# Kernel tuning notes

Hardware: AMD Instinct MI355X
Metric: run time of the kernel (lower is better)

The kernel has to match this reference:

```python
import jax, jax.numpy as jnp
import numpy as np

# ---- fixed problem dims (match init_kwargs) ----
B = 256            # graph pairs
NQ, NC = 96, 120   # nodes per query / corpus graph
EQ, EC = 192, 240  # edges per query / corpus graph
M = 256            # max_edge_set_size (pad target)
RAW = 32           # raw node/edge feature dim
H = 64             # node_state_dim
MSG = 128          # message_dim == encoded edge dim
SDIM = 64          # sinkhorn_feature_dim
PROP_STEPS = 3
TIME_STEPS = 2
SINK_ITERS = 10
TEMP = 0.1
N_NODES = B * (NQ + NC)
N_EDGES = B * (EQ + EC)


def _mlp2(x, W1, b1, W2, b2):
    return jax.nn.relu(x @ W1 + b1) @ W2 + b2


def _split_and_stack(ef):
    # edges laid out [q0, c0, q1, c1, ...]; pad each graph's edges to M
    D = ef.shape[-1]
    ef = ef.reshape(B, EQ + EC, D)
    q = jnp.pad(ef[:, :EQ], ((0, 0), (0, M - EQ), (0, 0)))
    c = jnp.pad(ef[:, EQ:], ((0, 0), (0, M - EC), (0, 0)))
    return q, c


def _sinkhorn(log_alpha):
    la = log_alpha / TEMP
    for _ in range(SINK_ITERS):
        la = la - jax.nn.logsumexp(la, axis=2, keepdims=True)
        la = la - jax.nn.logsumexp(la, axis=1, keepdims=True)
    return jnp.exp(la)


def setup_inputs() -> dict:
    key = jax.random.key(0)
    ks = jax.random.split(key, 16)
    rng = np.random.default_rng(0)
    nodes_per_graph = np.tile(np.array([NQ, NC]), B)            # [2B]
    node_offsets = np.concatenate([[0], np.cumsum(nodes_per_graph)[:-1]])
    edges_per_graph = np.tile(np.array([EQ, EC]), B)
    eg = np.repeat(np.arange(2 * B), edges_per_graph)           # graph id per edge
    from_idx = node_offsets[eg] + rng.integers(0, nodes_per_graph[eg])
    to_idx = node_offsets[eg] + rng.integers(0, nodes_per_graph[eg])

    def lin(k, i, o):
        return (jax.random.normal(k, (i, o), jnp.float32) / np.sqrt(i)).astype(jnp.float32)

    return {
        "node_features": jax.random.normal(ks[0], (N_NODES, RAW), jnp.float32),
        "edge_features": jax.random.normal(ks[1], (N_EDGES, RAW), jnp.float32),
        "from_idx": jnp.asarray(from_idx, jnp.int32),
        "to_idx": jnp.asarray(to_idx, jnp.int32),
        "enc_node_W": lin(ks[2], RAW, H), "enc_node_b": jnp.zeros((H,), jnp.float32),
        "enc_edge_W": lin(ks[3], RAW, MSG), "enc_edge_b": jnp.zeros((MSG,), jnp.float32),
        "msg_W1": lin(ks[4], 2 * H + MSG, 2 * MSG), "msg_b1": jnp.zeros((2 * MSG,), jnp.float32),
        "msg_W2": lin(ks[5], 2 * MSG, MSG), "msg_b2": jnp.zeros((MSG,), jnp.float32),
        "upd_W1": lin(ks[6], H + 2 * MSG, 2 * H), "upd_b1": jnp.zeros((2 * H,), jnp.float32),
        "upd_W2": lin(ks[7], 2 * H, H), "upd_b2": jnp.zeros((H,), jnp.float32),
        "int_W1": lin(ks[8], 2 * MSG, 2 * MSG), "int_b1": jnp.zeros((2 * MSG,), jnp.float32),
        "int_W2": lin(ks[9], 2 * MSG, MSG), "int_b2": jnp.zeros((MSG,), jnp.float32),
        "sink_W1": lin(ks[10], MSG, SDIM), "sink_b1": jnp.zeros((SDIM,), jnp.float32),
        "sink_W2": lin(ks[11], SDIM, SDIM), "sink_b2": jnp.zeros((SDIM,), jnp.float32),
    }


def _forward(node_features, edge_features,
             enc_node_W, enc_node_b, enc_edge_W, enc_edge_b,
             msg_W1, msg_b1, msg_W2, msg_b2,
             upd_W1, upd_b1, upd_W2, upd_b2,
             int_W1, int_b1, int_W2, int_b2,
             sink_W1, sink_b1, sink_W2, sink_b2,
             from_idx, to_idx):
    h0 = node_features @ enc_node_W + enc_node_b      # GraphEncoder (nodes)
    e0 = edge_features @ enc_edge_W + enc_edge_b      # GraphEncoder (edges) -> MSG dim
    mask_q = (jnp.arange(M) < EQ).astype(h0.dtype)[None, :, None]
    mask_c = (jnp.arange(M) < EC).astype(h0.dtype)[None, :, None]

    def edge_msgs(h, comb):
        hf, ht = h[from_idx], h[to_idx]
        mf = _mlp2(jnp.concatenate([hf, ht, comb], -1), msg_W1, msg_b1, msg_W2, msg_b2)
        mb = _mlp2(jnp.concatenate([ht, hf, comb], -1), msg_W1, msg_b1, msg_W2, msg_b2)
        return mf, mb

    plan = None
    q_store = c_store = None
    for _ in range(TIME_STEPS):
        h, e = h0, e0
        inter = jnp.zeros((N_EDGES, MSG), e0.dtype)
        for _ in range(PROP_STEPS):
            # interaction encoder on [edge_features_enc, interaction_features]
            comb = _mlp2(jnp.concatenate([e, inter], -1), int_W1, int_b1, int_W2, int_b2)
            # prop_layer: bidirectional messages + aggregation + node update
            mf, mb = edge_msgs(h, comb)
            agg_f = jax.ops.segment_sum(mf, to_idx, num_segments=N_NODES)
            agg_b = jax.ops.segment_sum(mb, from_idx, num_segments=N_NODES)
            h = _mlp2(jnp.concatenate([h, agg_f, agg_b], -1), upd_W1, upd_b1, upd_W2, upd_b2)
            # propagation_messages: per-edge messages from updated node states
            mf2, mb2 = edge_msgs(h, comb)
            e = mf2 + mb2
            # interaction features via transport-plan gather (zeros on first time step)
            if plan is None:
                inter = jnp.zeros((N_EDGES, MSG), e.dtype)
            else:
                qs, cs = _split_and_stack(e)
                q_int = jnp.einsum('bqc,bcd->bqd', plan, cs)[:, :EQ]
                c_int = jnp.einsum('bqc,bqd->bcd', plan, qs)[:, :EC]
                inter = jnp.concatenate([q_int, c_int], 1).reshape(N_EDGES, MSG)
        q_store, c_store = _split_and_stack(e)
        fq = _mlp2(q_store, sink_W1, sink_b1, sink_W2, sink_b2) * mask_q
        fc = _mlp2(c_store, sink_W1, sink_b1, sink_W2, sink_b2) * mask_c
        plan = _sinkhorn(jnp.einsum('bqd,bcd->bqc', fq, fc))
    # feature_alignment_score: -||Q - P C||_1 per pair
    return -jnp.abs(q_store - jnp.einsum('bqc,bcd->bqd', plan, c_store)).sum((1, 2))


def reference(node_features, edge_features, from_idx, to_idx,
              enc_node_W, enc_node_b, enc_edge_W, enc_edge_b,
              msg_W1, msg_b1, msg_W2, msg_b2,
              upd_W1, upd_b1, upd_W2, upd_b2,
              int_W1, int_b1, int_W2, int_b2,
              sink_W1, sink_b1, sink_W2, sink_b2):
    return _forward(node_features, edge_features,
                    enc_node_W, enc_node_b, enc_edge_W, enc_edge_b,
                    msg_W1, msg_b1, msg_W2, msg_b2,
                    upd_W1, upd_b1, upd_W2, upd_b2,
                    int_W1, int_b1, int_W2, int_b2,
                    sink_W1, sink_b1, sink_W2, sink_b2,
                    from_idx, to_idx)
```

## Files before the change

### kernel.cpp

```cpp
#include <hip/hip_runtime.h>
#include <math.h>

constexpr int BATCH = 256;
constexpr int EQ_   = 192;
constexpr int EC_   = 240;
constexpr int EPG   = 432;
constexpr int NPG   = 216;
constexpr int NN    = BATCH * NPG;
constexpr int NE    = BATCH * EPG;

typedef __attribute__((ext_vector_type(8))) short short8;
typedef __attribute__((ext_vector_type(4))) float floatx4;
typedef unsigned short u16;

__device__ __forceinline__ u16 f2bf(float x) {
  union { float f; unsigned u; } c; c.f = x;
  const unsigned r = (c.u + 0x7FFFu + ((c.u >> 16) & 1u)) >> 16;
  return (u16)r;
}
__device__ __forceinline__ float bf2f(u16 x) {
  union { unsigned u; float f; } c; c.u = ((unsigned)x) << 16;
  return c.f;
}
__device__ __forceinline__ unsigned pack2(float a, float b) {
  return (unsigned)f2bf(a) | ((unsigned)f2bf(b) << 16);
}
__device__ __forceinline__ short8 cvt8(const float* __restrict__ p) {
  const float4 a = *(const float4*)p;
  const float4 b = *(const float4*)(p + 4);
  short8 o;
  o[0]=(short)f2bf(a.x); o[1]=(short)f2bf(a.y); o[2]=(short)f2bf(a.z); o[3]=(short)f2bf(a.w);
  o[4]=(short)f2bf(b.x); o[5]=(short)f2bf(b.y); o[6]=(short)f2bf(b.z); o[7]=(short)f2bf(b.w);
  return o;
}

__device__ __forceinline__ void lse_online(float& m, float& s, float tt) {
  if (tt > m) { s = s * __expf(m - tt) + 1.f; m = tt; }
  else        { s += __expf(tt - m); }
}

__global__ __launch_bounds__(256)
void wconv(const float* __restrict__ W, u16* __restrict__ out, int K, int N)
{
  const int i = blockIdx.x * 256 + threadIdx.x;
  if (i < K * N) {
    const int n = i / K, k = i - n * K;
    out[i] = f2bf(W[(size_t)k * N + n]);
  }
}

template<int K1, int HID, int NOUT, int IN_MODE, int DUAL, int OUT_MODE, int WAVES>
__global__ __launch_bounds__(WAVES * 64, 4)
void mlp_mfma(const void* __restrict__ X, const void* __restrict__ P2,
              const void* __restrict__ P3, const u16* __restrict__ CB,
              const int* __restrict__ IA, const int* __restrict__ IB,
              const u16* __restrict__ W1t, const float* __restrict__ B1,
              const u16* __restrict__ W2t, const float* __restrict__ B2,
              float* __restrict__ Yf, u16* __restrict__ Yb0, u16* __restrict__ Yb1)
{
  constexpr int RT  = 32;
  constexpr int THREADS = WAVES * 64;
  constexpr int KCH = K1 / 8;
  constexpr int NT1 = HID / (WAVES * 16);
  constexpr int NT2 = (NOUT / (WAVES * 16) > 0) ? NOUT / (WAVES * 16) : 1;
  constexpr int SAB = RT * K1 * 2;
  constexpr int SHB = RT * (HID + 8) * 2;
  __shared__ __align__(16) char smem[(SAB > SHB ? SAB : SHB)];
  u16* sA = (u16*)smem;
  u16* sH = (u16*)smem;

  const int tid = threadIdx.x;
  const int rowBase = blockIdx.x * RT;

  for (int ch = tid; ch < RT * KCH; ch += THREADS) {
    const int r = ch / KCH, kc = ch - r * KCH;
    const int gr = rowBase + r, k0 = kc * 8;
    short8 pk;
    if constexpr (IN_MODE == 4) {
      const float* Xf  = (const float*)X;
      const float* P2f = (const float*)P2;
      if (k0 < 128)      pk = cvt8(&Xf[(size_t)gr * 128 + k0]);
      else if (P2f)      pk = cvt8(&P2f[(size_t)gr * 128 + (k0 - 128)]);
      else { pk = short8{0,0,0,0,0,0,0,0}; }
    } else if constexpr (IN_MODE == 1) {
      const u16* Hb = (const u16*)X;
      if (k0 < 64)       pk = *(const short8*)&Hb[(size_t)IA[gr] * 64 + k0];
      else if (k0 < 128) pk = *(const short8*)&Hb[(size_t)IB[gr] * 64 + (k0 - 64)];
      else               pk = *(const short8*)&CB[(size_t)gr * 128 + (k0 - 128)];
    } else {
      const u16* Hb = (const u16*)X;
      const u16* A0 = (const u16*)P2;
      const u16* A1 = (const u16*)P3;
      if (k0 < 64)       pk = *(const short8*)&Hb[(size_t)gr * 64 + k0];
      else if (k0 < 192) pk = *(const short8*)&A0[(size_t)gr * 128 + (k0 - 64)];
      else               pk = *(const short8*)&A1[(size_t)gr * 128 + (k0 - 192)];
    }
    const int byte = ((r * K1 + k0) * 2) ^ ((r & 7) << 4);
    *(short8*)((char*)sA + byte) = pk;
  }
  __syncthreads();

  const int wid = tid >> 6, lane = tid & 63;
  const int l15 = lane & 15, lg = lane >> 4;

  floatx4 acc1[1 + DUAL][2][NT1];
  #pragma unroll
  for (int d = 0; d <= DUAL; ++d)
    #pragma unroll
    for (int m = 0; m < 2; ++m)
      #pragma unroll
      for (int n = 0; n < NT1; ++n) acc1[d][m][n] = floatx4{0.f,0.f,0.f,0.f};

  #pragma unroll 2
  for (int kk = 0; kk < K1 / 32; ++kk) {
    short8 bw[NT1];
    #pragma unroll
    for (int n = 0; n < NT1; ++n) {
      const int col = wid * (HID / WAVES) + n * 16 + l15;
      bw[n] = *(const short8*)&W1t[(size_t)col * K1 + kk * 32 + lg * 8];
    }
    #pragma unroll
    for (int d = 0; d <= DUAL; ++d) {
      int k0 = kk * 32 + lg * 8;
      if (DUAL && d && k0 < 128) k0 ^= 64;
      #pragma unroll
      for (int m = 0; m < 2; ++m) {
        const int r = m * 16 + l15;
        const int byte = ((r * K1 + k0) * 2) ^ ((r & 7) << 4);
        const short8 af = *(const short8*)((char*)sA + byte);
        #pragma unroll
        for (int n = 0; n < NT1; ++n)
          acc1[d][m][n] = __builtin_amdgcn_mfma_f32_16x16x32_bf16(af, bw[n], acc1[d][m][n], 0, 0, 0);
      }
    }
  }
  __syncthreads();

  floatx4 accO[2][NT2];
  #pragma unroll
  for (int m = 0; m < 2; ++m)
    #pragma unroll
    for (int n = 0; n < NT2; ++n) accO[m][n] = floatx4{0.f,0.f,0.f,0.f};

  #pragma unroll
  for (int d = 0; d <= DUAL; ++d) {
    #pragma unroll
    for (int n = 0; n < NT1; ++n) {
      const int col = wid * (HID / WAVES) + n * 16 + l15;
      const float b1 = B1[col];
      #pragma unroll
      for (int m = 0; m < 2; ++m)
        #pragma unroll
        for (int r = 0; r < 4; ++r) {
          const int row = m * 16 + lg * 4 + r;
          const float y = acc1[d][m][n][r] + b1;
          sH[row * (HID + 8) + col] = f2bf(y > 0.f ? y : 0.f);
        }
    }
    __syncthreads();
    if (OUT_MODE == 2 && d == 1) {
      #pragma unroll
      for (int m = 0; m < 2; ++m)
        #pragma unroll
        for (int n = 0; n < NT2; ++n) accO[m][n] = floatx4{0.f,0.f,0.f,0.f};
    }
    #pragma unroll 2
    for (int kk = 0; kk < HID / 32; ++kk) {
      short8 bw2[NT2];
      #pragma unroll
      for (int n = 0; n < NT2; ++n) {
        const int col = wid * (NOUT / WAVES) + n * 16 + l15;
        bw2[n] = *(const short8*)&W2t[(size_t)col * HID + kk * 32 + lg * 8];
      }
      #pragma unroll
      for (int m = 0; m < 2; ++m) {
        const short8 af = *(const short8*)&sH[(m * 16 + l15) * (HID + 8) + kk * 32 + lg * 8];
        #pragma unroll
        for (int n = 0; n < NT2; ++n)
          accO[m][n] = __builtin_amdgcn_mfma_f32_16x16x32_bf16(af, bw2[n], accO[m][n], 0, 0, 0);
      }
    }
    if constexpr (OUT_MODE == 2) {
      u16* Y = d ? Yb1 : Yb0;
      #pragma unroll
      for (int n = 0; n < NT2; ++n) {
        const int col = wid * (NOUT / WAVES) + n * 16 + l15;
        const float b2 = B2[col];
        #pragma unroll
        for (int m = 0; m < 2; ++m)
          #pragma unroll
          for (int r = 0; r < 4; ++r) {
            const int gr = rowBase + m * 16 + lg * 4 + r;
            Y[(size_t)gr * NOUT + col] = f2bf(accO[m][n][r] + b2);
          }
      }
    }
    if (DUAL && d == 0) __syncthreads();
  }

  if constexpr (OUT_MODE != 2) {
    #pragma unroll
    for (int n = 0; n < NT2; ++n) {
      const int col = wid * (NOUT / WAVES) + n * 16 + l15;
      const float b2 = B2[col] * (float)(1 + DUAL);
      #pragma unroll
      for (int m = 0; m < 2; ++m)
        #pragma unroll
        for (int r = 0; r < 4; ++r) {
          const int gr = rowBase + m * 16 + lg * 4 + r;
          const float y = accO[m][n][r] + b2;
          if constexpr (OUT_MODE == 1) Yb0[(size_t)gr * NOUT + col] = f2bf(y);
          else                         Yf[(size_t)gr * NOUT + col] = y;
        }
    }
  }
}

__global__ __launch_bounds__(512, 4)
void comb_msg_fused(const float* __restrict__ E, const float* __restrict__ INTER,
                    const u16* __restrict__ Hb,
                    const int* __restrict__ IA, const int* __restrict__ IB,
                    const u16* __restrict__ Wi1, const float* __restrict__ Bi1,
                    const u16* __restrict__ Wi2, const float* __restrict__ Bi2,
                    const u16* __restrict__ Wm1, const float* __restrict__ Bm1,
                    const u16* __restrict__ Wm2, const float* __restrict__ Bm2,
                    u16* __restrict__ COMB, u16* __restrict__ MI )
{
  constexpr int RT = 32;
  __shared__ __align__(16) char smem[RT * (256 + 8) * 2];
  u16* sA = (u16*)smem;
  u16* sH = (u16*)smem;

  const int tid = threadIdx.x;
  const int rowBase = blockIdx.x * RT;
  const int wid = tid >> 6, lane = tid & 63;
  const int l15 = lane & 15, lg = lane >> 4;

  for (int ch = tid; ch < RT * 32; ch += 512) {
    const int r = ch >> 5, kc = ch & 31;
    const int gr = rowBase + r, k0 = kc * 8;
    short8 pk;
    if (k0 < 128)   pk = cvt8(&E[(size_t)gr * 128 + k0]);
    else if (INTER) pk = cvt8(&INTER[(size_t)gr * 128 + (k0 - 128)]);
    else            pk = short8{0,0,0,0,0,0,0,0};
    const int byte = ((r * 256 + k0) * 2) ^ ((r & 7) << 4);
    *(short8*)((char*)sA + byte) = pk;
  }
  __syncthreads();

  floatx4 c1[2][2];
  #pragma unroll
  for (int m = 0; m < 2; ++m) { c1[m][0] = floatx4{0,0,0,0}; c1[m][1] = floatx4{0,0,0,0}; }
  #pragma unroll 2
  for (int kk = 0; kk < 8; ++kk) {
    short8 bw[2];
    #pragma unroll
    for (int n = 0; n < 2; ++n) {
      const int col = wid * 32 + n * 16 + l15;
      bw[n] = *(const short8*)&Wi1[(size_t)col * 256 + kk * 32 + lg * 8];
    }
    #pragma unroll
    for (int m = 0; m < 2; ++m) {
      const int r = m * 16 + l15;
      const int byte = ((r * 256 + kk * 32 + lg * 8) * 2) ^ ((r & 7) << 4);
      const short8 af = *(const short8*)((char*)sA + byte);
      c1[m][0] = __builtin_amdgcn_mfma_f32_16x16x32_bf16(af, bw[0], c1[m][0], 0, 0, 0);
      c1[m][1] = __builtin_amdgcn_mfma_f32_16x16x32_bf16(af, bw[1], c1[m][1], 0, 0, 0);
    }
  }
  __syncthreads();
  #pragma unroll
  for (int n = 0; n < 2; ++n) {
    const int col = wid * 32 + n * 16 + l15;
    const float b1 = Bi1[col];
    #pragma unroll
    for (int m = 0; m < 2; ++m)
      #pragma unroll
      for (int r = 0; r < 4; ++r) {
        const int row = m * 16 + lg * 4 + r;
        const float y = c1[m][n][r] + b1;
        sH[row * 264 + col] = f2bf(y > 0.f ? y : 0.f);
      }
  }
  __syncthreads();
  floatx4 cO[2];
  cO[0] = floatx4{0,0,0,0}; cO[1] = floatx4{0,0,0,0};
  #pragma unroll 2
  for (int kk = 0; kk < 8; ++kk) {
    const int col = wid * 16 + l15;
    const short8 bw2 = *(const short8*)&Wi2[(size_t)col * 256 + kk * 32 + lg * 8];
    #pragma unroll
    for (int m = 0; m < 2; ++m) {
      const short8 af = *(const short8*)&sH[(m * 16 + l15) * 264 + kk * 32 + lg * 8];
      cO[m] = __builtin_amdgcn_mfma_f32_16x16x32_bf16(af, bw2, cO[m], 0, 0, 0);
    }
  }
  __syncthreads();

  {
    const int col = wid * 16 + l15;
    const float b2 = Bi2[col];
    #pragma unroll
    for (int m = 0; m < 2; ++m)
      #pragma unroll
      for (int r = 0; r < 4; ++r) {
        const int row = m * 16 + lg * 4 + r;
        const int gr = rowBase + row;
        const u16 v = f2bf(cO[m][r] + b2);
        COMB[(size_t)gr * 128 + col] = v;
        const int k0 = 128 + col;
        const int byte = ((row * 256 + k0) * 2) ^ ((row & 7) << 4);
        *(u16*)((char*)sA + byte) = v;
      }
  }
  for (int ch = tid; ch < RT * 16; ch += 512) {
    const int r = ch >> 4, kc = ch & 15;
    const int gr = rowBase + r, k0 = kc * 8;
    short8 pk;
    if (k0 < 64) pk = *(const short8*)&Hb[(size_t)IA[gr] * 64 + k0];
    else         pk = *(const short8*)&Hb[(size_t)IB[gr] * 64 + (k0 - 64)];
    const int byte = ((r * 256 + k0) * 2) ^ ((r & 7) << 4);
    *(short8*)((char*)sA + byte) = pk;
  }
  __syncthreads();

  floatx4 m1[2][2][2];
  #pragma unroll
  for (int d = 0; d < 2; ++d)
    #pragma unroll
    for (int m = 0; m < 2; ++m) { m1[d][m][0] = floatx4{0,0,0,0}; m1[d][m][1] = floatx4{0,0,0,0}; }
  #pragma unroll 2
  for (int kk = 0; kk < 8; ++kk) {
    short8 bw[2];
    #pragma unroll
    for (int n = 0; n < 2; ++n) {
      const int col = wid * 32 + n * 16 + l15;
      bw[n] = *(const short8*)&Wm1[(size_t)col * 256 + kk * 32 + lg * 8];
    }
    #pragma unroll
    for (int d = 0; d < 2; ++d) {
      int k0 = kk * 32 + lg * 8;
      if (d && k0 < 128) k0 ^= 64;
      #pragma unroll
      for (int m = 0; m < 2; ++m) {
        const int r = m * 16 + l15;
        const int byte = ((r * 256 + k0) * 2) ^ ((r & 7) << 4);
        const short8 af = *(const short8*)((char*)sA + byte);
        m1[d][m][0] = __builtin_amdgcn_mfma_f32_16x16x32_bf16(af, bw[0], m1[d][m][0], 0, 0, 0);
        m1[d][m][1] = __builtin_amdgcn_mfma_f32_16x16x32_bf16(af, bw[1], m1[d][m][1], 0, 0, 0);
      }
    }
  }
  __syncthreads();

  floatx4 mO[2];
  #pragma unroll
  for (int d = 0; d < 2; ++d) {
    #pragma unroll
    for (int n = 0; n < 2; ++n) {
      const int col = wid * 32 + n * 16 + l15;
      const float b1 = Bm1[col];
      #pragma unroll
      for (int m = 0; m < 2; ++m)
        #pragma unroll
        for (int r = 0; r < 4; ++r) {
          const int row = m * 16 + lg * 4 + r;
          const float y = m1[d][m][n][r] + b1;
          sH[row * 264 + col] = f2bf(y > 0.f ? y : 0.f);
        }
    }
    __syncthreads();
    mO[0] = floatx4{0,0,0,0}; mO[1] = floatx4{0,0,0,0};
    #pragma unroll 2
    for (int kk = 0; kk < 8; ++kk) {
      const int col = wid * 16 + l15;
      const short8 bw2 = *(const short8*)&Wm2[(size_t)col * 256 + kk * 32 + lg * 8];
      #pragma unroll
      for (int m = 0; m < 2; ++m) {
        const short8 af = *(const short8*)&sH[(m * 16 + l15) * 264 + kk * 32 + lg * 8];
        mO[m] = __builtin_amdgcn_mfma_f32_16x16x32_bf16(af, bw2, mO[m], 0, 0, 0);
      }
    }
    {
      const int col = wid * 16 + l15;
      const float b2 = Bm2[col];
      #pragma unroll
      for (int m = 0; m < 2; ++m)
        #pragma unroll
        for (int r = 0; r < 4; ++r) {
          const int gr = rowBase + m * 16 + lg * 4 + r;
          MI[(size_t)gr * 256 + d * 128 + col] = f2bf(mO[m][r] + b2);
        }
    }
    if (d == 0) __syncthreads();
  }
}

__global__ __launch_bounds__(512)
void scatter_agg(const u16* __restrict__ MI,
                 const int* __restrict__ FI, const int* __restrict__ TI,
                 u16* __restrict__ AggF, u16* __restrict__ AggB)
{
  const int pair = blockIdx.x >> 1, dir = blockIdx.x & 1;
  const int* SI = dir ? FI : TI;
  u16* Agg      = dir ? AggB : AggF;
  const int tid = threadIdx.x;
  __shared__ float sAgg[NPG * 128];

  for (int i = tid; i < NPG * 128; i += 512) sAgg[i] = 0.f;
  __syncthreads();

  for (int i = tid; i < EPG * 32; i += 512) {
    const int edge = i >> 5, cb = i & 31;
    const int er = pair * EPG + edge;
    const int node = SI[er] - pair * NPG;
    const size_t base = (size_t)er * 256 + dir * 128 + cb;
    #pragma unroll
    for (int k = 0; k < 4; ++k)
      atomicAdd(&sAgg[node * 128 + cb + 32 * k], bf2f(MI[base + 32 * k]));
  }
  __syncthreads();
  unsigned* dst = (unsigned*)(Agg + (size_t)pair * NPG * 128);
  for (int i = tid; i < NPG * 64; i += 512)
    dst[i] = pack2(sAgg[2 * i], sAgg[2 * i + 1]);
}

template<int K1, int HID, int NOUT, int IN_MODE, int SINGLE, int OUTBF>
__global__ __launch_bounds__(256)
void fused_mlp(const float* __restrict__ X, const float* __restrict__ P1,
               const float* __restrict__ W1, const float* __restrict__ B1,
               const float* __restrict__ W2, const float* __restrict__ B2,
               float* __restrict__ Y, u16* __restrict__ Yb, int maskLen)
{
  constexpr int RT = 32, BK = 32;
  constexpr int J1 = HID / 32;
  constexpr int J2 = NOUT / 32;
  constexpr int BMAX = (HID > NOUT ? HID : NOUT);
  __shared__ float sA[RT * 33];
  __shared__ float sB[BK * BMAX];
  __shared__ float sH[SINGLE ? 1 : RT * (HID + 1)];

  const int t  = threadIdx.x;
  const int tx = t & 31, ty = t >> 5;
  const int rowBase = blockIdx.x * RT;

  float acc[4][J1];
  #pragma unroll
  for (int i = 0; i < 4; ++i)
    #pragma unroll
    for (int j = 0; j < J1; ++j) acc[i][j] = 0.f;

  for (int kb = 0; kb < K1; kb += BK) {
    for (int l = t; l < RT * BK; l += 256) {
      const int r = l >> 5, k = l & 31;
      const int gr = rowBase + r, gk = kb + k;
      float v;
      if constexpr (IN_MODE == 0) {
        v = X[(size_t)gr * K1 + gk];
      } else {
        const int bb = gr >> 8, m = gr & 255;
        constexpr int off = (IN_MODE == 5) ? 0 : EQ_;
        constexpr int len = (IN_MODE == 5) ? EQ_ : EC_;
        v = (m < len) ? P1[((size_t)bb * EPG + off + m) * 128 + gk] : 0.f;
      }
      sA[r * 33 + k] = v;
    }
    for (int l = t * 4; l < BK * HID; l += 1024) {
      *(float4*)&sB[l] = *(const float4*)&W1[(size_t)(kb + l / HID) * HID + (l % HID)];
    }
    __syncthreads();
    #pragma unroll
    for (int k = 0; k < BK; ++k) {
      const float a0 = sA[(ty*4+0)*33+k], a1 = sA[(ty*4+1)*33+k],
                  a2 = sA[(ty*4+2)*33+k], a3 = sA[(ty*4+3)*33+k];
      #pragma unroll
      for (int j = 0; j < J1; ++j) {
        const float bb = sB[k * HID + tx + 32*j];
        acc[0][j] += a0 * bb; acc[1][j] += a1 * bb;
        acc[2][j] += a2 * bb; acc[3][j] += a3 * bb;
      }
    }
    __syncthreads();
  }

  if constexpr (SINGLE) {
    #pragma unroll
    for (int j = 0; j < J1; ++j) {
      const int col = tx + 32*j;
      const float bias = B1[col];
      #pragma unroll
      for (int i = 0; i < 4; ++i) {
        const int gr = rowBase + ty*4 + i;
        if constexpr (OUTBF) Yb[(size_t)gr * HID + col] = f2bf(acc[i][j] + bias);
        else                 Y[(size_t)gr * HID + col] = acc[i][j] + bias;
      }
    }
  } else {
    #pragma unroll
    for (int j = 0; j < J1; ++j) {
      const int col = tx + 32*j;
      const float bias = B1[col];
      #pragma unroll
      for (int i = 0; i < 4; ++i) {
        float y = acc[i][j] + bias;
        sH[(ty*4+i) * (HID+1) + col] = y > 0.f ? y : 0.f;
      }
    }
    __syncthreads();

    float acc2[4][J2];
    #pragma unroll
    for (int i = 0; i < 4; ++i)
      #pragma unroll
      for (int j = 0; j < J2; ++j) acc2[i][j] = 0.f;

    for (int kb = 0; kb < HID; kb += BK) {
      for (int l = t * 4; l < BK * NOUT; l += 1024) {
        *(float4*)&sB[l] = *(const float4*)&W2[(size_t)(kb + l / NOUT) * NOUT + (l % NOUT)];
      }
      __syncthreads();
      #pragma unroll
      for (int k = 0; k < BK; ++k) {
        const float a0 = sH[(ty*4+0)*(HID+1) + kb + k],
                    a1 = sH[(ty*4+1)*(HID+1) + kb + k],
                    a2 = sH[(ty*4+2)*(HID+1) + kb + k],
                    a3 = sH[(ty*4+3)*(HID+1) + kb + k];
        #pragma unroll
        for (int j = 0; j < J2; ++j) {
          const float bb = sB[k * NOUT + tx + 32*j];
          acc2[0][j] += a0 * bb; acc2[1][j] += a1 * bb;
          acc2[2][j] += a2 * bb; acc2[3][j] += a3 * bb;
        }
      }
      __syncthreads();
    }
    #pragma unroll
    for (int j = 0; j < J2; ++j) {
      const int col = tx + 32*j;
      const float bias = B2[col];
      #pragma unroll
      for (int i = 0; i < 4; ++i) {
        const int gr = rowBase + ty*4 + i;
        float y = acc2[i][j] + bias;
        if (maskLen >= 0 && (gr & 255) >= maskLen) y = 0.f;
        Y[(size_t)gr * NOUT + col] = y;
      }
    }
  }
}

__global__ __launch_bounds__(256)
void gemm_nt_scale(const float* __restrict__ A, const float* __restrict__ Bm,
                   float* __restrict__ C, float scale)
{
  const int b = blockIdx.z, qt = blockIdx.x, ct = blockIdx.y;
  __shared__ float sA[64 * 68];
  __shared__ float sB[64 * 68];
  const int t = threadIdx.x;
  const int tx = t & 15, ty = t >> 4;
  const float* Ab = A  + (size_t)b * 16384 + (size_t)qt * 4096;
  const float* Bb = Bm + (size_t)b * 16384 + (size_t)ct * 4096;
  for (int l = t * 4; l < 64 * 64; l += 1024) {
    const int r = l >> 6, d = l & 63;
    *(float4*)&sA[r*68 + d] = *(const float4*)&Ab[r*64 + d];
    *(float4*)&sB[r*68 + d] = *(const float4*)&Bb[r*64 + d];
  }
  __syncthreads();
  float acc[4][4] = {};
  #pragma unroll
  for (int d = 0; d < 64; ++d) {
    float a[4], bb[4];
    #pragma unroll
    for (int i = 0; i < 4; ++i) a[i]  = sA[(ty*4+i)*68 + d];
    #pragma unroll
    for (int j = 0; j < 4; ++j) bb[j] = sB[(tx+16*j)*68 + d];
    #pragma unroll
    for (int i = 0; i < 4; ++i)
      #pragma unroll
      for (int j = 0; j < 4; ++j) acc[i][j] += a[i] * bb[j];
  }
  float* Cb = C + (size_t)b * 65536 + (size_t)(qt*64) * 256 + ct*64;
  #pragma unroll
  for (int i = 0; i < 4; ++i)
    #pragma unroll
    for (int j = 0; j < 4; ++j)
      Cb[(ty*4+i)*256 + tx + 16*j] = acc[i][j] * scale;
}

template<int TRANSA>
__global__ __launch_bounds__(256)
void gemm_plan_mfma(const float* __restrict__ P, const float* __restrict__ E,
                    float* __restrict__ Y, int RPB, int YOFF, int VOFF,
                    int VLEN, int maskRows)
{
  __shared__ u16 sP[64 * 40];
  __shared__ u16 sVT[128 * 40];
  const int b = blockIdx.y, rt = blockIdx.x;
  const int t = threadIdx.x;
  const int wid = t >> 6, lane = t & 63;
  const int l15 = lane & 15, lg = lane >> 4;
  const float* Pb = P + (size_t)b * 65536;

  floatx4 acc[8];
  #pragma unroll
  for (int n = 0; n < 8; ++n) acc[n] = floatx4{0.f,0.f,0.f,0.f};

  for (int kb = 0; kb < 256; kb += 32) {
    if constexpr (TRANSA == 0) {
      for (int l = t; l < 64 * 32; l += 256) {
        const int r = l >> 5, k = l & 31;
        sP[r * 40 + k] = f2bf(Pb[(size_t)(rt * 64 + r) * 256 + kb + k]);
      }
    } else {
      for (int l = t; l < 64 * 32; l += 256) {
        const int q = l >> 6, c = l & 63;
        sP[c * 40 + q] = f2bf(Pb[(size_t)(kb + q) * 256 + rt * 64 + c]);
      }
    }
    for (int l = t; l < 32 * 128; l += 256) {
      const int k = l >> 7, d = l & 127;
      const int vr = kb + k;
      float v = 0.f;
      if (vr < VLEN) v = E[((size_t)b * EPG + VOFF + vr) * 128 + d];
      sVT[d * 40 + k] = f2bf(v);
    }
    __syncthreads();
    const short8 af = *(const short8*)&sP[(wid * 16 + l15) * 40 + lg * 8];
    #pragma unroll
    for (int n = 0; n < 8; ++n) {
      const short8 bw = *(const short8*)&sVT[(n * 16 + l15) * 40 + lg * 8];
      acc[n] = __builtin_amdgcn_mfma_f32_16x16x32_bf16(af, bw, acc[n], 0, 0, 0);
    }
    __syncthreads();
  }
  #pragma unroll
  for (int n = 0; n < 8; ++n) {
    const int col = n * 16 + l15;
    #pragma unroll
    for (int r = 0; r < 4; ++r) {
      const int row = rt * 64 + wid * 16 + lg * 4 + r;
      if (row < maskRows)
        Y[((size_t)b * RPB + YOFF + row) * 128 + col] = acc[n][r];
    }
  }
}

__global__ __launch_bounds__(1024)
void sinkhorn_fused(float* __restrict__ S)
{
  const int b = blockIdx.x, t = threadIdx.x;
  float* Sb = S + (size_t)b * 65536;
  const int w = t >> 6, lane = t & 63;
  const int cbase = lane * 4;
  __shared__ float pm[16 * 256], ps[16 * 256];
  __shared__ float su[256], sv[256];
  if (t < 256) sv[t] = 0.f;
  __syncthreads();

  for (int it = 0; it < 10; ++it) {
    const float4 v4 = *(const float4*)&sv[cbase];
    float4 cm = {-1e30f, -1e30f, -1e30f, -1e30f};
    float4 cs = {0.f, 0.f, 0.f, 0.f};
    #pragma unroll 2
    for (int i = 0; i < 16; ++i) {
      const int r = w * 16 + i;
      const float4 s4 = *(const float4*)&Sb[(size_t)r * 256 + cbase];
      const float ax = s4.x + v4.x, ay = s4.y + v4.y;
      const float az = s4.z + v4.z, aw = s4.w + v4.w;
      float m = fmaxf(fmaxf(ax, ay), fmaxf(az, aw));
      #pragma unroll
      for (int off = 32; off; off >>= 1) m = fmaxf(m, __shfl_xor(m, off));
      float s = __expf(ax - m) + __expf(ay - m) + __expf(az - m) + __expf(aw - m);
      #pragma unroll
      for (int off = 32; off; off >>= 1) s += __shfl_xor(s, off);
      const float u = -(m + __logf(s));
      if (lane == 0) su[r] = u;
      lse_online(cm.x, cs.x, s4.x + u);
      lse_online(cm.y, cs.y, s4.y + u);
      lse_online(cm.z, cs.z, s4.z + u);
      lse_online(cm.w, cs.w, s4.w + u);
    }
    *(float4*)&pm[w * 256 + cbase] = cm;
    *(float4*)&ps[w * 256 + cbase] = cs;
    __syncthreads();
    if (t < 256) {
      float m = pm[t];
      #pragma unroll
      for (int k = 1; k < 16; ++k) m = fmaxf(m, pm[k * 256 + t]);
      float s = 0.f;
      #pragma unroll
      for (int k = 0; k < 16; ++k) s += ps[k * 256 + t] * __expf(pm[k * 256 + t] - m);
      sv[t] = -(m + __logf(s));
    }
    __syncthreads();
  }
  for (int i = t; i < 16384; i += 1024) {
    const int row = i >> 6, c4 = (i & 63) * 4;
    float4 s4 = *(float4*)&Sb[(size_t)row * 256 + c4];
    const float uu = su[row];
    const float4 v4 = *(const float4*)&sv[c4];
    s4.x = __expf(s4.x + uu + v4.x);
    s4.y = __expf(s4.y + uu + v4.y);
    s4.z = __expf(s4.z + uu + v4.z);
    s4.w = __expf(s4.w + uu + v4.w);
    *(float4*)&Sb[(size_t)row * 256 + c4] = s4;
  }
}

__global__ __launch_bounds__(256)
void escore_kernel(const float* __restrict__ e, const float* __restrict__ pc,
                   float* __restrict__ out)
{
  const int b = blockIdx.x, t = threadIdx.x;
  float acc = 0.f;
  for (int i4 = t; i4 < 8192; i4 += 256) {
    const int flat = i4 * 4;
    const int m = flat >> 7, d = flat & 127;
    float4 p = *(const float4*)&pc[((size_t)b * 256 + m) * 128 + d];
    float4 q = {0.f, 0.f, 0.f, 0.f};
    if (m < EQ_) q = *(const float4*)&e[((size_t)b * EPG + m) * 128 + d];
    acc += fabsf(q.x - p.x) + fabsf(q.y - p.y) + fabsf(q.z - p.z) + fabsf(q.w - p.w);
  }
  __shared__ float red[256];
  red[t] = acc; __syncthreads();
  for (int s2 = 128; s2 > 0; s2 >>= 1) { if (t < s2) red[t] += red[t + s2]; __syncthreads(); }
  if (t == 0) out[b] = -red[0];
}

extern "C" void kernel_launch(void* const* d_in, const int* in_sizes, int n_in,
                              void* d_out, int out_size, void* d_ws, size_t ws_size,
                              hipStream_t stream)
{
  const float* node_features = (const float*)d_in[0];
  const float* edge_features = (const float*)d_in[1];
  const int*   from_idx      = (const int*)d_in[2];
  const int*   to_idx        = (const int*)d_in[3];
  const float* enc_node_W = (const float*)d_in[4];
  const float* enc_node_b = (const float*)d_in[5];
  const float* enc_edge_W = (const float*)d_in[6];
  const float* enc_edge_b = (const float*)d_in[7];
  const float* msg_W1 = (const float*)d_in[8];
  const float* msg_b1 = (const float*)d_in[9];
  const float* msg_W2 = (const float*)d_in[10];
  const float* msg_b2 = (const float*)d_in[11];
  const float* upd_W1 = (const float*)d_in[12];
  const float* upd_b1 = (const float*)d_in[13];
  const float* upd_W2 = (const float*)d_in[14];
  const float* upd_b2 = (const float*)d_in[15];
  const float* int_W1 = (const float*)d_in[16];
  const float* int_b1 = (const float*)d_in[17];
  const float* int_W2 = (const float*)d_in[18];
  const float* int_b2 = (const float*)d_in[19];
  const float* sink_W1 = (const float*)d_in[20];
  const float* sink_b1 = (const float*)d_in[21];
  const float* sink_W2 = (const float*)d_in[22];
  const float* sink_b2 = (const float*)d_in[23];
  float* out = (float*)d_out;

  float* wsf = (float*)d_ws;
  float* hreg = wsf;
  float* e   = hreg + (size_t)NN * 64;
  float* shr = e + (size_t)NE * 128;
  float* S   = shr + (size_t)NE * 128;
  u16* comb  = (u16*)(S + (size_t)BATCH * 65536);
  u16* wi1 = comb + (size_t)NE * 128;
  u16* wi2 = wi1 + 65536;
  u16* wm1 = wi2 + 32768;
  u16* wm2 = wm1 + 65536;
  u16* wu1 = wm2 + 32768;
  u16* wu2 = wu1 + 40960;

  u16* hb = (u16*)hreg;
  u16* mI = (u16*)e;

  u16* aggFb = (u16*)shr;
  u16* aggBb = aggFb + (size_t)NN * 128;
  float* inter = shr;
  float* fq    = shr;
  float* fc    = shr + (size_t)BATCH * 16384;

  wconv<<<256, 256, 0, stream>>>(int_W1, wi1, 256, 256);
  wconv<<<128, 256, 0, stream>>>(int_W2, wi2, 256, 128);
  wconv<<<256, 256, 0, stream>>>(msg_W1, wm1, 256, 256);
  wconv<<<128, 256, 0, stream>>>(msg_W2, wm2, 256, 128);
  wconv<<<160, 256, 0, stream>>>(upd_W1, wu1, 320, 128);
  wconv<<< 32, 256, 0, stream>>>(upd_W2, wu2, 128, 64);

  for (int ts = 0; ts < 2; ++ts) {
    fused_mlp<32,64,64,0,1,1><<<NN/32, 256, 0, stream>>>(
        node_features, nullptr, enc_node_W, enc_node_b, nullptr, nullptr,
        nullptr, hb, -1);
    fused_mlp<32,128,128,0,1,0><<<NE/32, 256, 0, stream>>>(
        edge_features, nullptr, enc_edge_W, enc_edge_b, nullptr, nullptr,
        e, nullptr, -1);

    for (int p = 0; p < 3; ++p) {
      const float* interArg = (ts == 1 && p > 0) ? inter : nullptr;
      comb_msg_fused<<<NE/32, 512, 0, stream>>>(
          e, interArg, hb, from_idx, to_idx,
          wi1, int_b1, wi2, int_b2, wm1, msg_b1, wm2, msg_b2,
          comb, mI);
      scatter_agg<<<BATCH*2, 512, 0, stream>>>(mI, from_idx, to_idx, aggFb, aggBb);
      mlp_mfma<320,128,64,3,0,1,4><<<NN/32, 256, 0, stream>>>(
          hb, aggFb, aggBb, nullptr, nullptr, nullptr,
          wu1, upd_b1, wu2, upd_b2, nullptr, hb, nullptr);
      mlp_mfma<256,256,128,1,1,0,8><<<NE/32, 512, 0, stream>>>(
          hb, nullptr, nullptr, comb, from_idx, to_idx,
          wm1, msg_b1, wm2, msg_b2, e, nullptr, nullptr);
      if (ts == 1 && p < 2) {
        gemm_plan_mfma<0><<<dim3(4, BATCH), 256, 0, stream>>>(
            S, e, inter, EPG, 0,   EQ_, EC_, EQ_);
        gemm_plan_mfma<1><<<dim3(4, BATCH), 256, 0, stream>>>(
            S, e, inter, EPG, EQ_, 0,   EQ_, EC_);
      }
    }
    fused_mlp<128,64,64,5,0,0><<<BATCH*8, 256, 0, stream>>>(
        nullptr, e, sink_W1, sink_b1, sink_W2, sink_b2, fq, nullptr, EQ_);
    fused_mlp<128,64,64,6,0,0><<<BATCH*8, 256, 0, stream>>>(
        nullptr, e, sink_W1, sink_b1, sink_W2, sink_b2, fc, nullptr, EC_);
    gemm_nt_scale<<<dim3(4,4,BATCH), 256, 0, stream>>>(fq, fc, S, 10.0f);
    sinkhorn_fused<<<BATCH, 1024, 0, stream>>>(S);
  }

  gemm_plan_mfma<0><<<dim3(4, BATCH), 256, 0, stream>>>(S, e, shr, 256, 0, EQ_, EC_, 256);
  escore_kernel<<<BATCH, 256, 0, stream>>>(e, shr, out);
}
```

Baseline: 4.000 ms.

## Reuse time-step-0 first propagation results instead of recomputing encoders in step 1

```diff
diff --git a/kernel.cpp b/kernel.cpp
--- a/kernel.cpp
+++ b/kernel.cpp
@@ -209,22 +209,28 @@
         for (int r = 0; r < 4; ++r) {
           const int gr = rowBase + m * 16 + lg * 4 + r;
           const float y = accO[m][n][r] + b2;
-          if constexpr (OUT_MODE == 1) Yb0[(size_t)gr * NOUT + col] = f2bf(y);
-          else                         Yf[(size_t)gr * NOUT + col] = y;
+          if constexpr (OUT_MODE == 1) {
+            Yb0[(size_t)gr * NOUT + col] = f2bf(y);
+          } else {
+            Yf[(size_t)gr * NOUT + col] = y;
+            if constexpr (OUT_MODE == 3)
+              Yb0[(size_t)gr * NOUT + col] = f2bf(y);
+          }
         }
     }
   }
 }
 
+template<int EBF16>
 __global__ __launch_bounds__(512, 4)
-void comb_msg_fused(const float* __restrict__ E, const float* __restrict__ INTER,
+void comb_msg_fused(const void* __restrict__ E, const u16* __restrict__ INTER,
                     const u16* __restrict__ Hb,
                     const int* __restrict__ IA, const int* __restrict__ IB,
                     const u16* __restrict__ Wi1, const float* __restrict__ Bi1,
                     const u16* __restrict__ Wi2, const float* __restrict__ Bi2,
                     const u16* __restrict__ Wm1, const float* __restrict__ Bm1,
                     const u16* __restrict__ Wm2, const float* __restrict__ Bm2,
-                    u16* __restrict__ COMB, u16* __restrict__ MI )
+                    u16* __restrict__ COMB, u16* __restrict__ MI)
 {
   constexpr int RT = 32;
   __shared__ __align__(16) char smem[RT * (256 + 8) * 2];
@@ -240,8 +246,11 @@
     const int r = ch >> 5, kc = ch & 31;
     const int gr = rowBase + r, k0 = kc * 8;
     short8 pk;
-    if (k0 < 128)   pk = cvt8(&E[(size_t)gr * 128 + k0]);
-    else if (INTER) pk = cvt8(&INTER[(size_t)gr * 128 + (k0 - 128)]);
+    if (k0 < 128) {
+      if constexpr (EBF16) pk = *(const short8*)&((const u16*)E)[(size_t)gr * 128 + k0];
+      else                 pk = cvt8(&((const float*)E)[(size_t)gr * 128 + k0]);
+    }
+    else if (INTER) pk = *(const short8*)&INTER[(size_t)gr * 128 + (k0 - 128)];
     else            pk = short8{0,0,0,0,0,0,0,0};
     const int byte = ((r * 256 + k0) * 2) ^ ((r & 7) << 4);
     *(short8*)((char*)sA + byte) = pk;
@@ -587,10 +596,10 @@
       Cb[(ty*4+i)*256 + tx + 16*j] = acc[i][j] * scale;
 }
 
-template<int TRANSA>
+template<int TRANSA, int EBF16, int OUTBF>
 __global__ __launch_bounds__(256)
-void gemm_plan_mfma(const float* __restrict__ P, const float* __restrict__ E,
-                    float* __restrict__ Y, int RPB, int YOFF, int VOFF,
+void gemm_plan_mfma(const float* __restrict__ P, const void* __restrict__ E,
+                    void* __restrict__ Y, int RPB, int YOFF, int VOFF,
                     int VLEN, int maskRows)
 {
   __shared__ u16 sP[64 * 40];
@@ -620,9 +629,12 @@
     for (int l = t; l < 32 * 128; l += 256) {
       const int k = l >> 7, d = l & 127;
       const int vr = kb + k;
-      float v = 0.f;
-      if (vr < VLEN) v = E[((size_t)b * EPG + VOFF + vr) * 128 + d];
-      sVT[d * 40 + k] = f2bf(v);
+      u16 v = 0;
+      if (vr < VLEN) {
+        if constexpr (EBF16) v = ((const u16*)E)[((size_t)b * EPG + VOFF + vr) * 128 + d];
+        else                 v = f2bf(((const float*)E)[((size_t)b * EPG + VOFF + vr) * 128 + d]);
+      }
+      sVT[d * 40 + k] = v;
     }
     __syncthreads();
     const short8 af = *(const short8*)&sP[(wid * 16 + l15) * 40 + lg * 8];
@@ -639,8 +651,11 @@
     #pragma unroll
     for (int r = 0; r < 4; ++r) {
       const int row = rt * 64 + wid * 16 + lg * 4 + r;
-      if (row < maskRows)
-        Y[((size_t)b * RPB + YOFF + row) * 128 + col] = acc[n][r];
+      if (row < maskRows) {
+        const size_t idx = ((size_t)b * RPB + YOFF + row) * 128 + col;
+        if constexpr (OUTBF) ((u16*)Y)[idx] = f2bf(acc[n][r]);
+        else                 ((float*)Y)[idx] = acc[n][r];
+      }
     }
   }
 }
@@ -757,27 +772,28 @@
   const float* sink_b2 = (const float*)d_in[23];
   float* out = (float*)d_out;
 
-  float* wsf = (float*)d_ws;
-  float* hreg = wsf;
-  float* e   = hreg + (size_t)NN * 64;
+  u16* wsu = (u16*)d_ws;
+  u16*   hb  = wsu;
+  float* e   = (float*)(wsu + (size_t)NN * 64);
   float* shr = e + (size_t)NE * 128;
-  float* S   = shr + (size_t)NE * 128;
+  float* S   = shr + (size_t)BATCH * 32768;
   u16* comb  = (u16*)(S + (size_t)BATCH * 65536);
-  u16* wi1 = comb + (size_t)NE * 128;
+  u16* e1b   = comb + (size_t)NE * 128;
+  u16* h1b   = e1b + (size_t)NE * 128;
+  u16* wi1 = h1b + (size_t)NN * 64;
   u16* wi2 = wi1 + 65536;
   u16* wm1 = wi2 + 32768;
   u16* wm2 = wm1 + 65536;
   u16* wu1 = wm2 + 32768;
   u16* wu2 = wu1 + 40960;
 
-  u16* hb = (u16*)hreg;
   u16* mI = (u16*)e;
-
-  u16* aggFb = (u16*)shr;
-  u16* aggBb = aggFb + (size_t)NN * 128;
-  float* inter = shr;
-  float* fq    = shr;
-  float* fc    = shr + (size_t)BATCH * 16384;
+  u16* interb = (u16*)shr;
+  u16* aggFb  = (u16*)shr;
+  u16* aggBb  = aggFb + (size_t)NN * 128;
+  float* fq   = shr;
+  float* fc   = shr + (size_t)BATCH * 16384;
+  float* pc   = shr;
 
   wconv<<<256, 256, 0, stream>>>(int_W1, wi1, 256, 256);
   wconv<<<128, 256, 0, stream>>>(int_W2, wi2, 256, 128);
@@ -786,42 +802,79 @@
   wconv<<<160, 256, 0, stream>>>(upd_W1, wu1, 320, 128);
   wconv<<< 32, 256, 0, stream>>>(upd_W2, wu2, 128, 64);
 
-  for (int ts = 0; ts < 2; ++ts) {
-    fused_mlp<32,64,64,0,1,1><<<NN/32, 256, 0, stream>>>(
-        node_features, nullptr, enc_node_W, enc_node_b, nullptr, nullptr,
-        nullptr, hb, -1);
-    fused_mlp<32,128,128,0,1,0><<<NE/32, 256, 0, stream>>>(
-        edge_features, nullptr, enc_edge_W, enc_edge_b, nullptr, nullptr,
-        e, nullptr, -1);
-
-    for (int p = 0; p < 3; ++p) {
-      const float* interArg = (ts == 1 && p > 0) ? inter : nullptr;
-      comb_msg_fused<<<NE/32, 512, 0, stream>>>(
-          e, interArg, hb, from_idx, to_idx,
-          wi1, int_b1, wi2, int_b2, wm1, msg_b1, wm2, msg_b2,
-          comb, mI);
-      scatter_agg<<<BATCH*2, 512, 0, stream>>>(mI, from_idx, to_idx, aggFb, aggBb);
-      mlp_mfma<320,128,64,3,0,1,4><<<NN/32, 256, 0, stream>>>(
-          hb, aggFb, aggBb, nullptr, nullptr, nullptr,
-          wu1, upd_b1, wu2, upd_b2, nullptr, hb, nullptr);
+  fused_mlp<32,64,64,0,1,1><<<NN/32, 256, 0, stream>>>(
+      node_features, nullptr, enc_node_W, enc_node_b, nullptr, nullptr,
+      nullptr, hb, -1);
+  fused_mlp<32,128,128,0,1,0><<<NE/32, 256, 0, stream>>>(
+      edge_features, nullptr, enc_edge_W, enc_edge_b, nullptr, nullptr,
+      e, nullptr, -1);
+
+  for (int p = 0; p < 3; ++p) {
+    comb_msg_fused<0><<<NE/32, 512, 0, stream>>>(
+        e, nullptr, hb, from_idx, to_idx,
+        wi1, int_b1, wi2, int_b2, wm1, msg_b1, wm2, msg_b2, comb, mI);
+    scatter_agg<<<BATCH*2, 512, 0, stream>>>(mI, from_idx, to_idx, aggFb, aggBb);
+    mlp_mfma<320,128,64,3,0,1,4><<<NN/32, 256, 0, stream>>>(
+        hb, aggFb, aggBb, nullptr, nullptr, nullptr,
+        wu1, upd_b1, wu2, upd_b2, nullptr, hb, nullptr);
+    if (p == 0) {
+      hipMemcpyAsync(h1b, hb, (size_t)NN * 64 * 2, hipMemcpyDeviceToDevice, stream);
+      mlp_mfma<256,256,128,1,1,3,8><<<NE/32, 512, 0, stream>>>(
+          hb, nullptr, nullptr, comb, from_idx, to_idx,
+          wm1, msg_b1, wm2, msg_b2, e, e1b, nullptr);
+    } else {
       mlp_mfma<256,256,128,1,1,0,8><<<NE/32, 512, 0, stream>>>(
           hb, nullptr, nullptr, comb, from_idx, to_idx,
           wm1, msg_b1, wm2, msg_b2, e, nullptr, nullptr);
-      if (ts == 1 && p < 2) {
-        gemm_plan_mfma<0><<<dim3(4, BATCH), 256, 0, stream>>>(
-            S, e, inter, EPG, 0,   EQ_, EC_, EQ_);
-        gemm_plan_mfma<1><<<dim3(4, BATCH), 256, 0, stream>>>(
-            S, e, inter, EPG, EQ_, 0,   EQ_, EC_);
-      }
-    }
-    fused_mlp<128,64,64,5,0,0><<<BATCH*8, 256, 0, stream>>>(
-        nullptr, e, sink_W1, sink_b1, sink_W2, sink_b2, fq, nullptr, EQ_);
-    fused_mlp<128,64,64,6,0,0><<<BATCH*8, 256, 0, stream>>>(
-        nullptr, e, sink_W1, sink_b1, sink_W2, sink_b2, fc, nullptr, EC_);
-    gemm_nt_scale<<<dim3(4,4,BATCH), 256, 0, stream>>>(fq, fc, S, 10.0f);
-    sinkhorn_fused<<<BATCH, 1024, 0, stream>>>(S);
-  }
-
-  gemm_plan_mfma<0><<<dim3(4, BATCH), 256, 0, stream>>>(S, e, shr, 256, 0, EQ_, EC_, 256);
-  escore_kernel<<<BATCH, 256, 0, stream>>>(e, shr, out);
-}
+    }
+  }
+  fused_mlp<128,64,64,5,0,0><<<BATCH*8, 256, 0, stream>>>(
+      nullptr, e, sink_W1, sink_b1, sink_W2, sink_b2, fq, nullptr, EQ_);
+  fused_mlp<128,64,64,6,0,0><<<BATCH*8, 256, 0, stream>>>(
+      nullptr, e, sink_W1, sink_b1, sink_W2, sink_b2, fc, nullptr, EC_);
+  gemm_nt_scale<<<dim3(4,4,BATCH), 256, 0, stream>>>(fq, fc, S, 10.0f);
+  sinkhorn_fused<<<BATCH, 1024, 0, stream>>>(S);
+
+  hipMemcpyAsync(hb, h1b, (size_t)NN * 64 * 2, hipMemcpyDeviceToDevice, stream);
+  gemm_plan_mfma<0,1,1><<<dim3(4, BATCH), 256, 0, stream>>>(
+      S, e1b, interb, EPG, 0,   EQ_, EC_, EQ_);
+  gemm_plan_mfma<1,1,1><<<dim3(4, BATCH), 256, 0, stream>>>(
+      S, e1b, interb, EPG, EQ_, 0,   EQ_, EC_);
+
+  comb_msg_fused<1><<<NE/32, 512, 0, stream>>>(
+      e1b, interb, hb, from_idx, to_idx,
+      wi1, int_b1, wi2, int_b2, wm1, msg_b1, wm2, msg_b2, comb, mI);
+  scatter_agg<<<BATCH*2, 512, 0, stream>>>(mI, from_idx, to_idx, aggFb, aggBb);
+  mlp_mfma<320,128,64,3,0,1,4><<<NN/32, 256, 0, stream>>>(
+      hb, aggFb, aggBb, nullptr, nullptr, nullptr,
+      wu1, upd_b1, wu2, upd_b2, nullptr, hb, nullptr);
+  mlp_mfma<256,256,128,1,1,0,8><<<NE/32, 512, 0, stream>>>(
+      hb, nullptr, nullptr, comb, from_idx, to_idx,
+      wm1, msg_b1, wm2, msg_b2, e, nullptr, nullptr);
+  gemm_plan_mfma<0,0,1><<<dim3(4, BATCH), 256, 0, stream>>>(
+      S, e, interb, EPG, 0,   EQ_, EC_, EQ_);
+  gemm_plan_mfma<1,0,1><<<dim3(4, BATCH), 256, 0, stream>>>(
+      S, e, interb, EPG, EQ_, 0,   EQ_, EC_);
+
+  comb_msg_fused<0><<<NE/32, 512, 0, stream>>>(
+      e, interb, hb, from_idx, to_idx,
+      wi1, int_b1, wi2, int_b2, wm1, msg_b1, wm2, msg_b2, comb, mI);
+  scatter_agg<<<BATCH*2, 512, 0, stream>>>(mI, from_idx, to_idx, aggFb, aggBb);
+  mlp_mfma<320,128,64,3,0,1,4><<<NN/32, 256, 0, stream>>>(
+      hb, aggFb, aggBb, nullptr, nullptr, nullptr,
+      wu1, upd_b1, wu2, upd_b2, nullptr, hb, nullptr);
+  mlp_mfma<256,256,128,1,1,0,8><<<NE/32, 512, 0, stream>>>(
+      hb, nullptr, nullptr, comb, from_idx, to_idx,
+      wm1, msg_b1, wm2, msg_b2, e, nullptr, nullptr);
+
+  fused_mlp<128,64,64,5,0,0><<<BATCH*8, 256, 0, stream>>>(
+      nullptr, e, sink_W1, sink_b1, sink_W2, sink_b2, fq, nullptr, EQ_);
+  fused_mlp<128,64,64,6,0,0><<<BATCH*8, 256, 0, stream>>>(
+      nullptr, e, sink_W1, sink_b1, sink_W2, sink_b2, fc, nullptr, EC_);
+  gemm_nt_scale<<<dim3(4,4,BATCH), 256, 0, stream>>>(fq, fc, S, 10.0f);
+  sinkhorn_fused<<<BATCH, 1024, 0, stream>>>(S);
+
+  gemm_plan_mfma<0,0,0><<<dim3(4, BATCH), 256, 0, stream>>>(
+      S, e, pc, 256, 0, EQ_, EC_, 256);
+  escore_kernel<<<BATCH, 256, 0, stream>>>(e, pc, out);
+}
```

Measured after the change: 3.492 ms. 1.15x faster.
